# Kernel tuning notes

Measured on AMD Instinct MI355X. Metric: run time of the kernel, lower is better.

The kernel has to match this reference:

```python
import jax, jax.numpy as jnp
import numpy as np

B, S, EPG = 1024, 64, 256          # graphs, nodes per graph, edges per graph
N, E = B * S, B * EPG              # 65536 nodes, 262144 edges
D, H = 128, 4                      # hidden dim, attention heads
DH = D // H
INIT_DIM, EDGE_DIM = 9, 3
N_EXTRA = 3                        # n_layers - 1
NEG_SLOPE = 0.2


def _gatv2(x, src, dst, edge_attr, Wl, Wr, bl, br, We, att, bias, heads, out_dim, concat):
    # PyG GATv2Conv with edge features: m = leaky_relu(xl[src]+xr[dst]+We@e),
    # alpha = segment_softmax(<m,att>, dst), out = scatter_add(alpha*xl[src], dst)
    n = x.shape[0]
    xl = (x @ Wl + bl).reshape(n, heads, out_dim)
    xr = (x @ Wr + br).reshape(n, heads, out_dim)
    ee = (edge_attr @ We).reshape(-1, heads, out_dim)
    m = jax.nn.leaky_relu(xl[src] + xr[dst] + ee, NEG_SLOPE)      # [E,H,O]
    logit = (m * att[None]).sum(-1)                               # [E,H]
    mx = jax.ops.segment_max(logit, dst, num_segments=n)
    ex = jnp.exp(logit - mx[dst])
    den = jax.ops.segment_sum(ex, dst, num_segments=n)
    alpha = ex / den[dst]                                         # segment softmax over in-edges
    out = jax.ops.segment_sum(xl[src] * alpha[:, :, None], dst, num_segments=n)
    out = out.reshape(n, heads * out_dim) if concat else out.mean(axis=1)
    return out + bias


def _forward(x, edge_index, edge_attr,
             g0_Wl, g0_Wr, g0_bl, g0_br, g0_We, g0_att, g0_bias,
             gWl, gWr, gbl, gbr, gWe, gatt, gbias,
             Wq, Wk, Wv, bq, bk, bv, Wo, bo):
    src, dst = edge_index[0], edge_index[1]
    h = _gatv2(x, src, dst, edge_attr, g0_Wl, g0_Wr, g0_bl, g0_br, g0_We, g0_att, g0_bias, 1, D, True)
    for i in range(N_EXTRA):
        h = (_gatv2(jax.nn.relu(h), src, dst, edge_attr,
                    gWl[i], gWr[i], gbl[i], gbr[i], gWe[i], gatt[i], gbias[i],
                    H, D, False) + h) / 2
    # to_dense_batch: equal-size graphs -> exact reshape, mask all True
    xd = h.reshape(B, S, D)
    q = (xd @ Wq + bq).reshape(B, S, H, DH)
    k = (xd @ Wk + bk).reshape(B, S, H, DH)
    v = (xd @ Wv + bv).reshape(B, S, H, DH)
    att = jax.nn.softmax(jnp.einsum('bqhd,bkhd->bhqk', q, k) / np.float32(np.sqrt(DH)), axis=-1)
    o = jnp.einsum('bhqk,bkhd->bqhd', att, v).reshape(B, S, D) @ Wo + bo
    return (h + o.reshape(N, D)) / 2


def setup_inputs():
    key = jax.random.key(0)
    ks = jax.random.split(key, 16)

    def gl(k, shape, fan):
        return jax.random.normal(k, shape, jnp.float32) / np.float32(np.sqrt(fan))

    x = jax.random.normal(ks[0], (N, INIT_DIM), jnp.float32)
    # random intra-graph edges: local indices in [0,S) offset per graph
    local = jax.random.randint(ks[1], (2, B, EPG), 0, S)
    edge_index = (local + (jnp.arange(B) * S)[None, :, None]).reshape(2, E)
    edge_attr = jax.random.normal(ks[2], (E, EDGE_DIM), jnp.float32)
    batch = jnp.repeat(jnp.arange(B), S)
    return dict(
        x=x, edge_index=edge_index, edge_attr=edge_attr, batch=batch,
        g0_Wl=gl(ks[3], (INIT_DIM, D), INIT_DIM), g0_Wr=gl(ks[4], (INIT_DIM, D), INIT_DIM),
        g0_bl=jnp.zeros((D,), jnp.float32), g0_br=jnp.zeros((D,), jnp.float32),
        g0_We=gl(ks[5], (EDGE_DIM, D), EDGE_DIM), g0_att=gl(ks[6], (1, D), D),
        g0_bias=jnp.zeros((D,), jnp.float32),
        gWl=gl(ks[7], (N_EXTRA, D, H * D), D), gWr=gl(ks[8], (N_EXTRA, D, H * D), D),
        gbl=jnp.zeros((N_EXTRA, H * D), jnp.float32), gbr=jnp.zeros((N_EXTRA, H * D), jnp.float32),
        gWe=gl(ks[9], (N_EXTRA, EDGE_DIM, H * D), EDGE_DIM), gatt=gl(ks[10], (N_EXTRA, H, D), D),
        gbias=jnp.zeros((N_EXTRA, D), jnp.float32),
        Wq=gl(ks[11], (D, D), D), Wk=gl(ks[12], (D, D), D), Wv=gl(ks[13], (D, D), D),
        bq=jnp.zeros((D,), jnp.float32), bk=jnp.zeros((D,), jnp.float32), bv=jnp.zeros((D,), jnp.float32),
        Wo=gl(ks[14], (D, D), D), bo=jnp.zeros((D,), jnp.float32),
    )


def reference(x, edge_index, edge_attr, batch,
              g0_Wl, g0_Wr, g0_bl, g0_br, g0_We, g0_att, g0_bias,
              gWl, gWr, gbl, gbr, gWe, gatt, gbias,
              Wq, Wk, Wv, bq, bk, bv, Wo, bo):
    # batch is implied by the equal-graph layout (reshape in _forward)
    return _forward(x, edge_index, edge_attr,
                    g0_Wl, g0_Wr, g0_bl, g0_br, g0_We, g0_att, g0_bias,
                    gWl, gWr, gbl, gbr, gWe, gatt, gbias,
                    Wq, Wk, Wv, bq, bk, bv, Wo, bo)
```

## Files before the change

kernel.cpp:

```cpp
#include <hip/hip_runtime.h>

constexpr int Bg  = 1024;
constexpr int Sg  = 64;
constexpr int EPG = 256;
constexpr int Nn  = Bg * Sg;
constexpr int Ne  = Bg * EPG;
constexpr int NH  = 4;
constexpr float NEG = 0.2f;

constexpr int CHUNK_G = 512;
constexpr int CHUNK_N = CHUNK_G * Sg;

typedef float  f32x4  __attribute__((ext_vector_type(4)));
typedef short  s16x8  __attribute__((ext_vector_type(8)));
typedef unsigned short u16x4 __attribute__((ext_vector_type(4)));

static __device__ __forceinline__ unsigned fenc(float f) {
    unsigned u = __float_as_uint(f);
    return (u & 0x80000000u) ? ~u : (u | 0x80000000u);
}
static __device__ __forceinline__ float fdec(unsigned k) {
    unsigned u = (k & 0x80000000u) ? (k ^ 0x80000000u) : ~k;
    return __uint_as_float(u);
}
static __device__ __forceinline__ unsigned short bf16rn(float x) {
    unsigned u = __float_as_uint(x);
    u += 0x7FFFu + ((u >> 16) & 1u);
    return (unsigned short)(u >> 16);
}
static __device__ __forceinline__ float bf16f(unsigned short h) {
    return __uint_as_float((unsigned)h << 16);
}

__global__ __launch_bounds__(256)
void wprep(const float* __restrict__ gWl, const float* __restrict__ gWr,
           const float* __restrict__ Wq, const float* __restrict__ Wk,
           const float* __restrict__ Wv, const float* __restrict__ Wo,
           unsigned short* __restrict__ whi, unsigned short* __restrict__ wlo) {
    int gid = blockIdx.x, t = threadIdx.x;
    const float* src;
    int n, k;
    size_t oidx;
    if (gid < 1536) {
        int s = gid >> 8;
        int e = ((gid & 255) << 8) + t;
        n = e & 511; k = e >> 9;
        src = (s & 1) ? (gWr + (s >> 1) * 65536) : (gWl + (s >> 1) * 65536);
        oidx = (size_t)s * 65536 + n * 128 + k;
        float v = src[k * 512 + n];
        unsigned short h = bf16rn(v);
        whi[oidx] = h;
        wlo[oidx] = bf16rn(v - bf16f(h));
    } else {
        int g2 = gid - 1536;
        int s = g2 >> 6;
        int e = ((g2 & 63) << 8) + t;
        n = e & 127; k = e >> 7;
        src = (s == 0) ? Wq : (s == 1) ? Wk : (s == 2) ? Wv : Wo;
        oidx = 393216 + (size_t)s * 16384 + n * 128 + k;
        float v = src[k * 128 + n];
        unsigned short h = bf16rn(v);
        whi[oidx] = h;
        wlo[oidx] = bf16rn(v - bf16f(h));
    }
}

__global__ __launch_bounds__(256)
void proj0(const float* __restrict__ x, const float* __restrict__ Wl,
           const float* __restrict__ Wr, const float* __restrict__ bl,
           const float* __restrict__ br, float* __restrict__ xl0,
           float* __restrict__ xr0) {
    int t = blockIdx.x * 256 + threadIdx.x;
    int n = t >> 7, j = t & 127;
    float xv[9];
#pragma unroll
    for (int k = 0; k < 9; ++k) xv[k] = x[n * 9 + k];
    float al = bl[j], ar = br[j];
#pragma unroll
    for (int k = 0; k < 9; ++k) {
        al = fmaf(xv[k], Wl[k * 128 + j], al);
        ar = fmaf(xv[k], Wr[k * 128 + j], ar);
    }
    xl0[t] = al;
    xr0[t] = ar;
}

template<bool RELU, int EPI>
__global__ __launch_bounds__(256, 2)
void gemm_mfma(const float* __restrict__ A, const unsigned short* __restrict__ wth,
               const unsigned short* __restrict__ wtl, const float* __restrict__ bias,
               const float* __restrict__ res, float* __restrict__ C, int NC) {
    __shared__ __align__(16) char smem[65536];
    constexpr int AH = 0, AL = 16384, BH = 32768, BL = 49152;

    const int t = threadIdx.x;
    const int r0 = blockIdx.y * 128, c0 = blockIdx.x * 128;
    const int wave = t >> 6, lane = t & 63;
    const int wm = wave >> 1, wn = wave & 1;
    const int lr = lane & 15, lg = lane >> 4;

    f32x4 acc[4][4] = {};

    int rowA[4], rowB[4];
#pragma unroll
    for (int i = 0; i < 4; ++i) {
        rowA[i] = wm * 64 + i * 16 + lr;
        rowB[i] = wn * 64 + i * 16 + lr;
    }

    for (int kc = 0; kc < 2; ++kc) {
#pragma unroll
        for (int i = 0; i < 8; ++i) {
            int f = t + i * 256;
            int row = f >> 4;
            int c4  = (f & 15) << 2;
            float4 v = *reinterpret_cast<const float4*>(
                &A[(size_t)(r0 + row) * 128 + kc * 64 + c4]);
            if (RELU) {
                v.x = fmaxf(v.x, 0.f); v.y = fmaxf(v.y, 0.f);
                v.z = fmaxf(v.z, 0.f); v.w = fmaxf(v.w, 0.f);
            }
            unsigned short h0 = bf16rn(v.x), h1 = bf16rn(v.y),
                           h2 = bf16rn(v.z), h3 = bf16rn(v.w);
            u16x4 hp = {h0, h1, h2, h3};
            u16x4 lp = {bf16rn(v.x - bf16f(h0)), bf16rn(v.y - bf16f(h1)),
                        bf16rn(v.z - bf16f(h2)), bf16rn(v.w - bf16f(h3))};
            int off = row * 128 + ((c4 * 2) ^ ((row & 7) << 4));
            *reinterpret_cast<u16x4*>(smem + AH + off) = hp;
            *reinterpret_cast<u16x4*>(smem + AL + off) = lp;
        }
#pragma unroll
        for (int i = 0; i < 4; ++i) {
            int f = t + i * 256;
            int row = f >> 3;
            int c8  = (f & 7) << 3;
            size_t gsrc = (size_t)(c0 + row) * 128 + kc * 64 + c8;
            s16x8 hv = *reinterpret_cast<const s16x8*>(&wth[gsrc]);
            s16x8 lv = *reinterpret_cast<const s16x8*>(&wtl[gsrc]);
            int off = row * 128 + ((c8 * 2) ^ ((row & 7) << 4));
            *reinterpret_cast<s16x8*>(smem + BH + off) = hv;
            *reinterpret_cast<s16x8*>(smem + BL + off) = lv;
        }
        __syncthreads();

#pragma unroll
        for (int ks = 0; ks < 2; ++ks) {
            const int kb = ks * 64 + lg * 16;
            s16x8 ah[4], al4[4];
#pragma unroll
            for (int mi = 0; mi < 4; ++mi) {
                int off = rowA[mi] * 128 + (kb ^ ((rowA[mi] & 7) << 4));
                ah[mi]  = *reinterpret_cast<const s16x8*>(smem + AH + off);
                al4[mi] = *reinterpret_cast<const s16x8*>(smem + AL + off);
            }
#pragma unroll
            for (int ni = 0; ni < 4; ++ni) {
                int off = rowB[ni] * 128 + (kb ^ ((rowB[ni] & 7) << 4));
                s16x8 bh = *reinterpret_cast<const s16x8*>(smem + BH + off);
                s16x8 bl = *reinterpret_cast<const s16x8*>(smem + BL + off);
#pragma unroll
                for (int mi = 0; mi < 4; ++mi) {
                    acc[mi][ni] = __builtin_amdgcn_mfma_f32_16x16x32_bf16(
                        ah[mi], bh, acc[mi][ni], 0, 0, 0);
                    acc[mi][ni] = __builtin_amdgcn_mfma_f32_16x16x32_bf16(
                        ah[mi], bl, acc[mi][ni], 0, 0, 0);
                    acc[mi][ni] = __builtin_amdgcn_mfma_f32_16x16x32_bf16(
                        al4[mi], bh, acc[mi][ni], 0, 0, 0);
                }
            }
        }
        __syncthreads();
    }

#pragma unroll
    for (int ni = 0; ni < 4; ++ni) {
        int c = c0 + wn * 64 + ni * 16 + lr;
        float bs = bias[c];
#pragma unroll
        for (int mi = 0; mi < 4; ++mi) {
#pragma unroll
            for (int j = 0; j < 4; ++j) {
                int r = r0 + wm * 64 + mi * 16 + lg * 4 + j;
                float ov = acc[mi][ni][j] + bs;
                if (EPI == 1) ov = (ov + res[(size_t)r * 128 + c]) * 0.5f;
                C[(size_t)r * NC + c] = ov;
            }
        }
    }
}

template<int HEADS, int EPI>
__global__ __launch_bounds__(512, 4)
void gat_edge(const float* __restrict__ xl, const float* __restrict__ xr,
              const int* __restrict__ ei, const float* __restrict__ ea,
              const float* __restrict__ We, const float* __restrict__ att,
              const float* __restrict__ bias, const float* __restrict__ hres,
              float* __restrict__ hout, int g0) {
    constexpr int WROW = HEADS * 128;
    constexpr int PST  = 68;
    __shared__ __align__(16) float xls[64 * 128];
    __shared__ __align__(16) float xrp[64 * 128];
    __shared__ float eas[EPG * 4];
    __shared__ float logit[EPG];
    __shared__ int   se[EPG], de[EPG];
    __shared__ unsigned nmax[64];
    __shared__ float nden[64];

    const int g = g0 + blockIdx.x;
    const int t = threadIdx.x, lane = t & 63, wave = t >> 6;
    const int rg = (t >> 5) << 2;
    const int cg = (t & 31) << 2;

    if (t < EPG) {
        se[t] = ei[g * EPG + t] - g * 64;
        de[t] = ei[Ne + g * EPG + t] - g * 64;
        eas[t * 4 + 0] = ea[(size_t)(g * EPG + t) * 3 + 0];
        eas[t * 4 + 1] = ea[(size_t)(g * EPG + t) * 3 + 1];
        eas[t * 4 + 2] = ea[(size_t)(g * EPG + t) * 3 + 2];
    }

    float acc[4][4] = {};

    for (int hh = 0; hh < HEADS; ++hh) {
        __syncthreads();
#pragma unroll
        for (int i = 0; i < 4; ++i) {
            int f  = t + i * 512;
            int r  = f >> 5;
            int c4 = (f & 31) << 2;
            size_t nl = (size_t)((g - g0) * 64 + r);
            *reinterpret_cast<float4*>(&xls[r * 128 + c4]) =
                *reinterpret_cast<const float4*>(&xl[nl * WROW + hh * 128 + c4]);
            *reinterpret_cast<float4*>(&xrp[r * 128 + c4]) =
                *reinterpret_cast<const float4*>(&xr[nl * WROW + hh * 128 + c4]);
        }
        if (t < 64) { nmax[t] = 0u; nden[t] = 0.f; }
        __syncthreads();

        const float a1 = att[hh * 128 + lane];
        const float a2 = att[hh * 128 + 64 + lane];
        float we1[3], we2[3];
#pragma unroll
        for (int k = 0; k < 3; ++k) {
            we1[k] = We[k * WROW + hh * 128 + lane];
            we2[k] = We[k * WROW + hh * 128 + 64 + lane];
        }

        for (int e = wave; e < EPG; e += 8) {
            int s_ = se[e], d_ = de[e];
            float e0 = eas[e * 4 + 0], e1 = eas[e * 4 + 1], e2 = eas[e * 4 + 2];
            float m1 = xls[s_ * 128 + lane] + xrp[d_ * 128 + lane]
                       + e0 * we1[0] + e1 * we1[1] + e2 * we1[2];
            float m2 = xls[s_ * 128 + 64 + lane] + xrp[d_ * 128 + 64 + lane]
                       + e0 * we2[0] + e1 * we2[1] + e2 * we2[2];
            m1 = m1 > 0.f ? m1 : NEG * m1;
            m2 = m2 > 0.f ? m2 : NEG * m2;
            float r = fmaf(m1, a1, m2 * a2);
#pragma unroll
            for (int o = 32; o; o >>= 1) r += __shfl_xor(r, o, 64);
            if (lane == 0) logit[e] = r;
        }
        __syncthreads();

        float* P = xrp;
        for (int i = t; i < 64 * PST; i += 512) P[i] = 0.f;
        if (t < EPG) atomicMax(&nmax[de[t]], fenc(logit[t]));
        __syncthreads();
        float ex = 0.f;
        if (t < EPG) {
            ex = __expf(logit[t] - fdec(nmax[de[t]]));
            atomicAdd(&nden[de[t]], ex);
        }
        __syncthreads();
        if (t < EPG) atomicAdd(&P[se[t] * PST + de[t]], ex / nden[de[t]]);
        __syncthreads();

#pragma unroll 4
        for (int k = 0; k < 64; ++k) {
            float4 pv = *reinterpret_cast<const float4*>(&P[k * PST + rg]);
            float4 xv = *reinterpret_cast<const float4*>(&xls[k * 128 + cg]);
            acc[0][0] = fmaf(pv.x, xv.x, acc[0][0]);
            acc[0][1] = fmaf(pv.x, xv.y, acc[0][1]);
            acc[0][2] = fmaf(pv.x, xv.z, acc[0][2]);
            acc[0][3] = fmaf(pv.x, xv.w, acc[0][3]);
            acc[1][0] = fmaf(pv.y, xv.x, acc[1][0]);
            acc[1][1] = fmaf(pv.y, xv.y, acc[1][1]);
            acc[1][2] = fmaf(pv.y, xv.z, acc[1][2]);
            acc[1][3] = fmaf(pv.y, xv.w, acc[1][3]);
            acc[2][0] = fmaf(pv.z, xv.x, acc[2][0]);
            acc[2][1] = fmaf(pv.z, xv.y, acc[2][1]);
            acc[2][2] = fmaf(pv.z, xv.z, acc[2][2]);
            acc[2][3] = fmaf(pv.z, xv.w, acc[2][3]);
            acc[3][0] = fmaf(pv.w, xv.x, acc[3][0]);
            acc[3][1] = fmaf(pv.w, xv.y, acc[3][1]);
            acc[3][2] = fmaf(pv.w, xv.z, acc[3][2]);
            acc[3][3] = fmaf(pv.w, xv.w, acc[3][3]);
        }
    }

    constexpr float inv = 1.0f / (float)HEADS;
#pragma unroll
    for (int i = 0; i < 4; ++i) {
        int r = rg + i;
        size_t gi = (size_t)(g * 64 + r) * 128 + cg;
        float4 v;
        v.x = acc[i][0] * inv + bias[cg + 0];
        v.y = acc[i][1] * inv + bias[cg + 1];
        v.z = acc[i][2] * inv + bias[cg + 2];
        v.w = acc[i][3] * inv + bias[cg + 3];
        if (EPI == 1) {
            const float4 rr = *reinterpret_cast<const float4*>(&hres[gi]);
            v.x = (v.x + rr.x) * 0.5f; v.y = (v.y + rr.y) * 0.5f;
            v.z = (v.z + rr.z) * 0.5f; v.w = (v.w + rr.w) * 0.5f;
        }
        *reinterpret_cast<float4*>(&hout[gi]) = v;
    }
}

__global__ __launch_bounds__(256, 3)
void attn_k(const float* __restrict__ q, const float* __restrict__ k,
            const float* __restrict__ v, float* __restrict__ o) {
    __shared__ __align__(16) float qT[32 * 68];
    __shared__ __align__(16) float kT[32 * 68];
    __shared__ __align__(16) float vs[64 * 36];
    __shared__ __align__(16) float St[64 * 68];
    __shared__ float rden[64];

    const int g = blockIdx.x >> 2, hh = blockIdx.x & 3;
    const int t = threadIdx.x;

#pragma unroll
    for (int i = 0; i < 2; ++i) {
        int f = t + i * 256;
        int row = f >> 3;
        int c4  = (f & 7) << 2;
        size_t gi = (size_t)(g * 64 + row) * 128 + hh * 32 + c4;
        float4 qv = *reinterpret_cast<const float4*>(&q[gi]);
        float4 kv = *reinterpret_cast<const float4*>(&k[gi]);
        float4 vv = *reinterpret_cast<const float4*>(&v[gi]);
        qT[(c4 + 0) * 68 + row] = qv.x; qT[(c4 + 1) * 68 + row] = qv.y;
        qT[(c4 + 2) * 68 + row] = qv.z; qT[(c4 + 3) * 68 + row] = qv.w;
        kT[(c4 + 0) * 68 + row] = kv.x; kT[(c4 + 1) * 68 + row] = kv.y;
        kT[(c4 + 2) * 68 + row] = kv.z; kT[(c4 + 3) * 68 + row] = kv.w;
        *reinterpret_cast<float4*>(&vs[row * 36 + c4]) = vv;
    }
    __syncthreads();

    {
        const int rg = (t & 15) << 2, cg = (t >> 4) << 2;
        float acc[4][4] = {};
#pragma unroll 8
        for (int kk = 0; kk < 32; ++kk) {
            float4 qv = *reinterpret_cast<const float4*>(&qT[kk * 68 + rg]);
            float4 kv = *reinterpret_cast<const float4*>(&kT[kk * 68 + cg]);
            acc[0][0] = fmaf(qv.x, kv.x, acc[0][0]);
            acc[0][1] = fmaf(qv.x, kv.y, acc[0][1]);
            acc[0][2] = fmaf(qv.x, kv.z, acc[0][2]);
            acc[0][3] = fmaf(qv.x, kv.w, acc[0][3]);
            acc[1][0] = fmaf(qv.y, kv.x, acc[1][0]);
            acc[1][1] = fmaf(qv.y, kv.y, acc[1][1]);
            acc[1][2] = fmaf(qv.y, kv.z, acc[1][2]);
            acc[1][3] = fmaf(qv.y, kv.w, acc[1][3]);
            acc[2][0] = fmaf(qv.z, kv.x, acc[2][0]);
            acc[2][1] = fmaf(qv.z, kv.y, acc[2][1]);
            acc[2][2] = fmaf(qv.z, kv.z, acc[2][2]);
            acc[2][3] = fmaf(qv.z, kv.w, acc[2][3]);
            acc[3][0] = fmaf(qv.w, kv.x, acc[3][0]);
            acc[3][1] = fmaf(qv.w, kv.y, acc[3][1]);
            acc[3][2] = fmaf(qv.w, kv.z, acc[3][2]);
            acc[3][3] = fmaf(qv.w, kv.w, acc[3][3]);
        }
        constexpr float sc = 0.17677669529663687f;
#pragma unroll
        for (int j = 0; j < 4; ++j) {
            float4 sv;
            sv.x = acc[0][j] * sc; sv.y = acc[1][j] * sc;
            sv.z = acc[2][j] * sc; sv.w = acc[3][j] * sc;
            *reinterpret_cast<float4*>(&St[(cg + j) * 68 + rg]) = sv;
        }
    }
    __syncthreads();

    {
        const int r = t >> 2, q4 = t & 3;
        float mx = -3.4e38f;
#pragma unroll
        for (int i = 0; i < 16; ++i)
            mx = fmaxf(mx, St[(q4 * 16 + i) * 68 + r]);
        mx = fmaxf(mx, __shfl_xor(mx, 1, 64));
        mx = fmaxf(mx, __shfl_xor(mx, 2, 64));
        float sm = 0.f;
#pragma unroll
        for (int i = 0; i < 16; ++i) {
            int idx = (q4 * 16 + i) * 68 + r;
            float e = __expf(St[idx] - mx);
            St[idx] = e;
            sm += e;
        }
        sm += __shfl_xor(sm, 1, 64);
        sm += __shfl_xor(sm, 2, 64);
        if (q4 == 0) rden[r] = 1.f / sm;
    }
    __syncthreads();

    {
        const int rg = (t & 15) << 2, dg = (t >> 4) << 1;
        float a0 = 0.f, a1 = 0.f, a2 = 0.f, a3 = 0.f;
        float b0 = 0.f, b1 = 0.f, b2 = 0.f, b3 = 0.f;
#pragma unroll 8
        for (int kk = 0; kk < 64; ++kk) {
            float4 pv = *reinterpret_cast<const float4*>(&St[kk * 68 + rg]);
            float2 vv = *reinterpret_cast<const float2*>(&vs[kk * 36 + dg]);
            a0 = fmaf(pv.x, vv.x, a0); b0 = fmaf(pv.x, vv.y, b0);
            a1 = fmaf(pv.y, vv.x, a1); b1 = fmaf(pv.y, vv.y, b1);
            a2 = fmaf(pv.z, vv.x, a2); b2 = fmaf(pv.z, vv.y, b2);
            a3 = fmaf(pv.w, vv.x, a3); b3 = fmaf(pv.w, vv.y, b3);
        }
        float4 rd = *reinterpret_cast<const float4*>(&rden[rg]);
        float2 o0 = {a0 * rd.x, b0 * rd.x};
        float2 o1 = {a1 * rd.y, b1 * rd.y};
        float2 o2 = {a2 * rd.z, b2 * rd.z};
        float2 o3 = {a3 * rd.w, b3 * rd.w};
        size_t gb = (size_t)(g * 64 + rg) * 128 + hh * 32 + dg;
        *reinterpret_cast<float2*>(&o[gb])           = o0;
        *reinterpret_cast<float2*>(&o[gb + 128])     = o1;
        *reinterpret_cast<float2*>(&o[gb + 256])     = o2;
        *reinterpret_cast<float2*>(&o[gb + 384])     = o3;
    }
}

extern "C" void kernel_launch(void* const* d_in, const int* in_sizes, int n_in,
                              void* d_out, int out_size, void* d_ws, size_t ws_size,
                              hipStream_t stream) {
    const float* x     = (const float*)d_in[0];
    const int*   ei    = (const int*)d_in[1];
    const float* ea    = (const float*)d_in[2];
    const float* g0Wl  = (const float*)d_in[4];
    const float* g0Wr  = (const float*)d_in[5];
    const float* g0bl  = (const float*)d_in[6];
    const float* g0br  = (const float*)d_in[7];
    const float* g0We  = (const float*)d_in[8];
    const float* g0att = (const float*)d_in[9];
    const float* g0bias= (const float*)d_in[10];
    const float* gWl   = (const float*)d_in[11];
    const float* gWr   = (const float*)d_in[12];
    const float* gbl   = (const float*)d_in[13];
    const float* gbr   = (const float*)d_in[14];
    const float* gWe   = (const float*)d_in[15];
    const float* gatt  = (const float*)d_in[16];
    const float* gbias = (const float*)d_in[17];
    const float* Wq    = (const float*)d_in[18];
    const float* Wk    = (const float*)d_in[19];
    const float* Wv    = (const float*)d_in[20];
    const float* bq    = (const float*)d_in[21];
    const float* bk    = (const float*)d_in[22];
    const float* bv    = (const float*)d_in[23];
    const float* Wo    = (const float*)d_in[24];
    const float* bo    = (const float*)d_in[25];
    float* out = (float*)d_out;
    float* ws  = (float*)d_ws;

    float* h   = ws;
    float* xlb = ws + (size_t)Nn * 128;
    float* xrb = xlb + (size_t)CHUNK_N * 512;
    float* qb = xlb;
    float* kb = xlb + (size_t)Nn * 128;
    float* vb = xrb;
    float* ob = xrb + (size_t)Nn * 128;
    unsigned short* whi = (unsigned short*)(xrb + (size_t)CHUNK_N * 512);
    unsigned short* wlo = whi + 458752;

    wprep<<<1792, 256, 0, stream>>>(gWl, gWr, Wq, Wk, Wv, Wo, whi, wlo);

    proj0<<<Nn * 128 / 256, 256, 0, stream>>>(x, g0Wl, g0Wr, g0bl, g0br, xlb, xrb);
    gat_edge<1, 0><<<Bg, 512, 0, stream>>>(xlb, xrb, ei, ea, g0We, g0att,
                                           g0bias, nullptr, h, 0);

    for (int i = 0; i < 3; ++i) {
        for (int c = 0; c < 2; ++c) {
            const float* Ain = h + (size_t)c * CHUNK_N * 128;
            dim3 grid(512 / 128, CHUNK_N / 128);
            gemm_mfma<true, 0><<<grid, 256, 0, stream>>>(
                Ain, whi + (size_t)(2 * i) * 65536, wlo + (size_t)(2 * i) * 65536,
                gbl + i * 512, nullptr, xlb, 512);
            gemm_mfma<true, 0><<<grid, 256, 0, stream>>>(
                Ain, whi + (size_t)(2 * i + 1) * 65536, wlo + (size_t)(2 * i + 1) * 65536,
                gbr + i * 512, nullptr, xrb, 512);
            gat_edge<4, 1><<<CHUNK_G, 512, 0, stream>>>(
                xlb, xrb, ei, ea, gWe + (size_t)i * 3 * 512,
                gatt + (size_t)i * 4 * 128, gbias + i * 128, h, h, c * CHUNK_G);
        }
    }

    {
        dim3 grid(1, Nn / 128);
        gemm_mfma<false, 0><<<grid, 256, 0, stream>>>(h, whi + 393216, wlo + 393216,
                                                      bq, nullptr, qb, 128);
        gemm_mfma<false, 0><<<grid, 256, 0, stream>>>(h, whi + 409600, wlo + 409600,
                                                      bk, nullptr, kb, 128);
        gemm_mfma<false, 0><<<grid, 256, 0, stream>>>(h, whi + 425984, wlo + 425984,
                                                      bv, nullptr, vb, 128);
        attn_k<<<Bg * NH, 256, 0, stream>>>(qb, kb, vb, ob);
        gemm_mfma<false, 1><<<grid, 256, 0, stream>>>(ob, whi + 442368, wlo + 442368,
                                                      bo, h, out, 128);
    }
}
```

Measured before the change: 1.217 ms.

## Use split-bf16 MFMA for GAT edge aggregation and DPP wave reductions

The per-graph alpha-weighted aggregation (P^T @ xl) in gat_edge moves from scalar FMA to 16x16x32 bf16 MFMA. It uses a three-term hi/lo bf16 split to keep near-fp32 accuracy. The xl/xr tiles are stored in LDS as packed hi/lo bf16 pairs and P is transposed so rows follow destinations. The logit wave reduction uses DPP row ops instead of shuffles, and edge features load as a float4. This costs extra pack/unpack ALU work and strided LDS reads for the B operand, in exchange for removing the FMA-bound inner loop.

```diff
diff --git a/kernel.cpp b/kernel.cpp
--- a/kernel.cpp
+++ b/kernel.cpp
@@ -31,6 +31,21 @@
 static __device__ __forceinline__ float bf16f(unsigned short h) {
     return __uint_as_float((unsigned)h << 16);
 }
+static __device__ __forceinline__ unsigned pack32(float x) {
+    unsigned u  = __float_as_uint(x);
+    unsigned hb = u & 0xffff0000u;
+    float lof   = x - __uint_as_float(hb);
+    return hb | (__float_as_uint(lof) >> 16);
+}
+static __device__ __forceinline__ float up_hi(unsigned u) {
+    return __uint_as_float(u & 0xffff0000u);
+}
+static __device__ __forceinline__ float up_lo(unsigned u) {
+    return __uint_as_float(u << 16);
+}
+#define DPP_ADD(x, ctrl) \
+    ((x) + __int_as_float(__builtin_amdgcn_update_dpp( \
+        0, __float_as_int(x), (ctrl), 0xF, 0xF, true)))
 
 __global__ __launch_bounds__(256)
 void wprep(const float* __restrict__ gWl, const float* __restrict__ gWr,
@@ -197,9 +212,8 @@
               const float* __restrict__ bias, const float* __restrict__ hres,
               float* __restrict__ hout, int g0) {
     constexpr int WROW = HEADS * 128;
-    constexpr int PST  = 68;
-    __shared__ __align__(16) float xls[64 * 128];
-    __shared__ __align__(16) float xrp[64 * 128];
+    __shared__ __align__(16) unsigned xli[64 * 128];
+    __shared__ __align__(16) unsigned xri[64 * 128];
     __shared__ float eas[EPG * 4];
     __shared__ float logit[EPG];
     __shared__ int   se[EPG], de[EPG];
@@ -208,8 +222,8 @@
 
     const int g = g0 + blockIdx.x;
     const int t = threadIdx.x, lane = t & 63, wave = t >> 6;
-    const int rg = (t >> 5) << 2;
-    const int cg = (t & 31) << 2;
+    const int lr = lane & 15, lg = lane >> 4;
+    const int wm = wave >> 2, wn = wave & 3;
 
     if (t < EPG) {
         se[t] = ei[g * EPG + t] - g * 64;
@@ -219,7 +233,8 @@
         eas[t * 4 + 2] = ea[(size_t)(g * EPG + t) * 3 + 2];
     }
 
-    float acc[4][4] = {};
+    f32x4 acc[2][2] = {};
+    float* P32 = reinterpret_cast<float*>(xri);
 
     for (int hh = 0; hh < HEADS; ++hh) {
         __syncthreads();
@@ -229,41 +244,49 @@
             int r  = f >> 5;
             int c4 = (f & 31) << 2;
             size_t nl = (size_t)((g - g0) * 64 + r);
-            *reinterpret_cast<float4*>(&xls[r * 128 + c4]) =
-                *reinterpret_cast<const float4*>(&xl[nl * WROW + hh * 128 + c4]);
-            *reinterpret_cast<float4*>(&xrp[r * 128 + c4]) =
-                *reinterpret_cast<const float4*>(&xr[nl * WROW + hh * 128 + c4]);
+            float4 vl = *reinterpret_cast<const float4*>(&xl[nl * WROW + hh * 128 + c4]);
+            float4 vr = *reinterpret_cast<const float4*>(&xr[nl * WROW + hh * 128 + c4]);
+            uint4 pl = {pack32(vl.x), pack32(vl.y), pack32(vl.z), pack32(vl.w)};
+            uint4 pr = {pack32(vr.x), pack32(vr.y), pack32(vr.z), pack32(vr.w)};
+            *reinterpret_cast<uint4*>(&xli[r * 128 + c4]) = pl;
+            *reinterpret_cast<uint4*>(&xri[r * 128 + c4]) = pr;
         }
         if (t < 64) { nmax[t] = 0u; nden[t] = 0.f; }
         __syncthreads();
 
-        const float a1 = att[hh * 128 + lane];
-        const float a2 = att[hh * 128 + 64 + lane];
+        const float a1 = att[hh * 128 + 2 * lane];
+        const float a2 = att[hh * 128 + 2 * lane + 1];
         float we1[3], we2[3];
 #pragma unroll
         for (int k = 0; k < 3; ++k) {
-            we1[k] = We[k * WROW + hh * 128 + lane];
-            we2[k] = We[k * WROW + hh * 128 + 64 + lane];
+            we1[k] = We[k * WROW + hh * 128 + 2 * lane];
+            we2[k] = We[k * WROW + hh * 128 + 2 * lane + 1];
         }
 
         for (int e = wave; e < EPG; e += 8) {
             int s_ = se[e], d_ = de[e];
-            float e0 = eas[e * 4 + 0], e1 = eas[e * 4 + 1], e2 = eas[e * 4 + 2];
-            float m1 = xls[s_ * 128 + lane] + xrp[d_ * 128 + lane]
-                       + e0 * we1[0] + e1 * we1[1] + e2 * we1[2];
-            float m2 = xls[s_ * 128 + 64 + lane] + xrp[d_ * 128 + 64 + lane]
-                       + e0 * we2[0] + e1 * we2[1] + e2 * we2[2];
+            float4 ev = *reinterpret_cast<const float4*>(&eas[e * 4]);
+            uint2 ul = *reinterpret_cast<const uint2*>(&xli[s_ * 128 + 2 * lane]);
+            uint2 ur = *reinterpret_cast<const uint2*>(&xri[d_ * 128 + 2 * lane]);
+            float m1 = up_hi(ul.x) + up_lo(ul.x) + up_hi(ur.x) + up_lo(ur.x)
+                       + ev.x * we1[0] + ev.y * we1[1] + ev.z * we1[2];
+            float m2 = up_hi(ul.y) + up_lo(ul.y) + up_hi(ur.y) + up_lo(ur.y)
+                       + ev.x * we2[0] + ev.y * we2[1] + ev.z * we2[2];
             m1 = m1 > 0.f ? m1 : NEG * m1;
             m2 = m2 > 0.f ? m2 : NEG * m2;
             float r = fmaf(m1, a1, m2 * a2);
-#pragma unroll
-            for (int o = 32; o; o >>= 1) r += __shfl_xor(r, o, 64);
-            if (lane == 0) logit[e] = r;
-        }
-        __syncthreads();
-
-        float* P = xrp;
-        for (int i = t; i < 64 * PST; i += 512) P[i] = 0.f;
+            r = DPP_ADD(r, 0x111);
+            r = DPP_ADD(r, 0x112);
+            r = DPP_ADD(r, 0x114);
+            r = DPP_ADD(r, 0x118);
+            r = DPP_ADD(r, 0x142);
+            r = DPP_ADD(r, 0x143);
+            if (lane == 63) logit[e] = r;
+        }
+        __syncthreads();
+
+        for (int i = t; i < 1088; i += 512)
+            reinterpret_cast<float4*>(P32)[i] = float4{0.f, 0.f, 0.f, 0.f};
         if (t < EPG) atomicMax(&nmax[de[t]], fenc(logit[t]));
         __syncthreads();
         float ex = 0.f;
@@ -272,48 +295,68 @@
             atomicAdd(&nden[de[t]], ex);
         }
         __syncthreads();
-        if (t < EPG) atomicAdd(&P[se[t] * PST + de[t]], ex / nden[de[t]]);
-        __syncthreads();
-
-#pragma unroll 4
-        for (int k = 0; k < 64; ++k) {
-            float4 pv = *reinterpret_cast<const float4*>(&P[k * PST + rg]);
-            float4 xv = *reinterpret_cast<const float4*>(&xls[k * 128 + cg]);
-            acc[0][0] = fmaf(pv.x, xv.x, acc[0][0]);
-            acc[0][1] = fmaf(pv.x, xv.y, acc[0][1]);
-            acc[0][2] = fmaf(pv.x, xv.z, acc[0][2]);
-            acc[0][3] = fmaf(pv.x, xv.w, acc[0][3]);
-            acc[1][0] = fmaf(pv.y, xv.x, acc[1][0]);
-            acc[1][1] = fmaf(pv.y, xv.y, acc[1][1]);
-            acc[1][2] = fmaf(pv.y, xv.z, acc[1][2]);
-            acc[1][3] = fmaf(pv.y, xv.w, acc[1][3]);
-            acc[2][0] = fmaf(pv.z, xv.x, acc[2][0]);
-            acc[2][1] = fmaf(pv.z, xv.y, acc[2][1]);
-            acc[2][2] = fmaf(pv.z, xv.z, acc[2][2]);
-            acc[2][3] = fmaf(pv.z, xv.w, acc[2][3]);
-            acc[3][0] = fmaf(pv.w, xv.x, acc[3][0]);
-            acc[3][1] = fmaf(pv.w, xv.y, acc[3][1]);
-            acc[3][2] = fmaf(pv.w, xv.z, acc[3][2]);
-            acc[3][3] = fmaf(pv.w, xv.w, acc[3][3]);
+        if (t < EPG) atomicAdd(&P32[de[t] * 68 + se[t]], ex / nden[de[t]]);
+        __syncthreads();
+
+#pragma unroll
+        for (int ks = 0; ks < 2; ++ks) {
+            s16x8 bh[2], bl[2];
+#pragma unroll
+            for (int nt = 0; nt < 2; ++nt) {
+                int n = wn * 32 + nt * 16 + lr;
+                unsigned uu[8];
+#pragma unroll
+                for (int j = 0; j < 8; ++j)
+                    uu[j] = xli[(ks * 32 + lg * 8 + j) * 128 + n];
+#pragma unroll
+                for (int j = 0; j < 8; ++j) {
+                    bh[nt][j] = (short)(uu[j] >> 16);
+                    bl[nt][j] = (short)(uu[j] & 0xffffu);
+                }
+            }
+#pragma unroll
+            for (int mi = 0; mi < 2; ++mi) {
+                const float* pr = &P32[(wm * 32 + mi * 16 + lr) * 68 + ks * 32 + lg * 8];
+                float4 p0 = *reinterpret_cast<const float4*>(pr);
+                float4 p1 = *reinterpret_cast<const float4*>(pr + 4);
+                float pv[8] = {p0.x, p0.y, p0.z, p0.w, p1.x, p1.y, p1.z, p1.w};
+                s16x8 pah, pal;
+#pragma unroll
+                for (int j = 0; j < 8; ++j) {
+                    unsigned u = __float_as_uint(pv[j]);
+                    unsigned hb = u & 0xffff0000u;
+                    pah[j] = (short)(u >> 16);
+                    pal[j] = (short)(__float_as_uint(pv[j] - __uint_as_float(hb)) >> 16);
+                }
+#pragma unroll
+                for (int nt = 0; nt < 2; ++nt) {
+                    acc[mi][nt] = __builtin_amdgcn_mfma_f32_16x16x32_bf16(
+                        pah, bh[nt], acc[mi][nt], 0, 0, 0);
+                    acc[mi][nt] = __builtin_amdgcn_mfma_f32_16x16x32_bf16(
+                        pah, bl[nt], acc[mi][nt], 0, 0, 0);
+                    acc[mi][nt] = __builtin_amdgcn_mfma_f32_16x16x32_bf16(
+                        pal, bh[nt], acc[mi][nt], 0, 0, 0);
+                }
+            }
         }
     }
 
     constexpr float inv = 1.0f / (float)HEADS;
 #pragma unroll
-    for (int i = 0; i < 4; ++i) {
-        int r = rg + i;
-        size_t gi = (size_t)(g * 64 + r) * 128 + cg;
-        float4 v;
-        v.x = acc[i][0] * inv + bias[cg + 0];
-        v.y = acc[i][1] * inv + bias[cg + 1];
-        v.z = acc[i][2] * inv + bias[cg + 2];
-        v.w = acc[i][3] * inv + bias[cg + 3];
-        if (EPI == 1) {
-            const float4 rr = *reinterpret_cast<const float4*>(&hres[gi]);
-            v.x = (v.x + rr.x) * 0.5f; v.y = (v.y + rr.y) * 0.5f;
-            v.z = (v.z + rr.z) * 0.5f; v.w = (v.w + rr.w) * 0.5f;
-        }
-        *reinterpret_cast<float4*>(&hout[gi]) = v;
+    for (int mi = 0; mi < 2; ++mi) {
+#pragma unroll
+        for (int nt = 0; nt < 2; ++nt) {
+            int c_ = wn * 32 + nt * 16 + lr;
+            float bs = bias[c_];
+#pragma unroll
+            for (int j = 0; j < 4; ++j) {
+                int r_ = wm * 32 + mi * 16 + lg * 4 + j;
+                size_t gi = (size_t)(g * 64 + r_) * 128 + c_;
+                float v = acc[mi][nt][j] * inv + bs;
+                if (EPI == 1) v = (v + hres[gi]) * 0.5f;
+                hout[gi] = v;
+            }
+        }
     }
 }
 
@@ -422,10 +465,10 @@
         float2 o2 = {a2 * rd.z, b2 * rd.z};
         float2 o3 = {a3 * rd.w, b3 * rd.w};
         size_t gb = (size_t)(g * 64 + rg) * 128 + hh * 32 + dg;
-        *reinterpret_cast<float2*>(&o[gb])           = o0;
-        *reinterpret_cast<float2*>(&o[gb + 128])     = o1;
-        *reinterpret_cast<float2*>(&o[gb + 256])     = o2;
-        *reinterpret_cast<float2*>(&o[gb + 384])     = o3;
+        *reinterpret_cast<float2*>(&o[gb])       = o0;
+        *reinterpret_cast<float2*>(&o[gb + 128]) = o1;
+        *reinterpret_cast<float2*>(&o[gb + 256]) = o2;
+        *reinterpret_cast<float2*>(&o[gb + 384]) = o3;
     }
 }
 
```

Result: faster. 1.049 ms (-13.8%).
